# Kernel optimization log

Measured on AMD Instinct MI355X. Metric: run time of the kernel, lower is better.

Reference implementation:

```python
import jax, jax.numpy as jnp
import numpy as np

TOP_K = 2


def setup_inputs() -> dict:
    key = jax.random.key(0)
    ks = jax.random.split(key, 6)
    B, S, H, I, E = 2, 1024, 1024, 2048, 8
    s_h = 1.0 / np.sqrt(H)
    s_i = 1.0 / np.sqrt(I)
    return {
        "x": jax.random.normal(ks[0], (B, S, H), jnp.float32),
        "gate_w": jax.random.normal(ks[1], (H, E), jnp.float32) * s_h,
        "gate_b": jnp.zeros((E,), jnp.float32),
        "w1": jax.random.normal(ks[2], (E, H, I), jnp.float32) * s_h,
        "w3": jax.random.normal(ks[3], (E, H, I), jnp.float32) * s_h,
        "w2": jax.random.normal(ks[4], (E, I, H), jnp.float32) * s_i,
    }


def reference(x, gate_w, gate_b, w1, w3, w2):
    # Gating: softmax over experts, then top-k selection + renormalization.
    logits = jnp.einsum("bsh,he->bse", x, gate_w) + gate_b            # [B,S,E]
    probs = jax.nn.softmax(logits, axis=-1)
    topk_w, topk_idx = jax.lax.top_k(probs, TOP_K)                    # [B,S,K]
    topk_w = topk_w / jnp.sum(topk_w, axis=-1, keepdims=True)

    E = gate_w.shape[-1]
    # Per-token combine weight for each expert (0 if not routed there).
    # one_hot: [B,S,K,E] -> combine: [B,S,E]
    combine = jnp.sum(jax.nn.one_hot(topk_idx, E, dtype=x.dtype) * topk_w[..., None], axis=-2)

    # SwiGLU expert FFN: down(silu(gate(x)) * up(x)); dense-masked reference
    # (compute every expert on every token, weight by combine; math identical
    # to the original gather/scatter loop since combine is 0 off-route).
    out = jnp.zeros_like(x)
    for e in range(E):
        h = jax.nn.silu(x @ w1[e]) * (x @ w3[e])                      # [B,S,I]
        out = out + combine[..., e:e + 1] * (h @ w2[e])               # [B,S,H]
    return out
```

## Files before the change

kernel.cpp:

```cpp
#include <hip/hip_runtime.h>
#include <hip/hip_bf16.h>
#include <math.h>

typedef __attribute__((ext_vector_type(4))) float f32x4;
typedef __attribute__((ext_vector_type(8))) short bf16x8;

#define T_TOK 2048
#define H_DIM 1024
#define I_DIM 2048
#define E_NUM 8

__device__ inline unsigned short f2bf(float f) {
  union { float f; unsigned int u; } v; v.f = f;
  unsigned int r = v.u + 0x7fffu + ((v.u >> 16) & 1u);
  return (unsigned short)(r >> 16);
}
__device__ inline unsigned int pack2(float a, float b) {
  return (unsigned int)f2bf(a) | ((unsigned int)f2bf(b) << 16);
}

__device__ inline void gld16(const void* g, void* l) {
  __builtin_amdgcn_global_load_lds((const __attribute__((address_space(1))) void*)g,
                                   (__attribute__((address_space(3))) void*)l, 16, 0, 0);
}

__device__ inline void transpose_pair(const float* __restrict__ ip, unsigned short* __restrict__ op,
                                      int R, int C, int rp, int ct, char* smem)
{
  unsigned short (*tl)[66] = (unsigned short (*)[66])smem;
  int r0 = rp * 128, c0 = ct * 64;
  int tid = threadIdx.x;
  int rq = (tid >> 4) * 4;
  int c4 = (tid & 15) * 4;
  const float* b0 = ip + (size_t)(r0 + rq) * C + c0 + c4;
  const float* b1 = b0 + (size_t)64 * C;
  float4 v[8];
  v[0] = *(const float4*)(b0);
  v[1] = *(const float4*)(b0 + C);
  v[2] = *(const float4*)(b0 + 2 * C);
  v[3] = *(const float4*)(b0 + 3 * C);
  v[4] = *(const float4*)(b1);
  v[5] = *(const float4*)(b1 + C);
  v[6] = *(const float4*)(b1 + 2 * C);
  v[7] = *(const float4*)(b1 + 3 * C);
  const float* f = (const float*)v;
#pragma unroll
  for (int j = 0; j < 4; ++j) {
    *(unsigned int*)&tl[c4 + j][rq]          = pack2(f[0 * 4 + j], f[1 * 4 + j]);
    *(unsigned int*)&tl[c4 + j][rq + 2]      = pack2(f[2 * 4 + j], f[3 * 4 + j]);
    *(unsigned int*)&tl[64 + c4 + j][rq]     = pack2(f[4 * 4 + j], f[5 * 4 + j]);
    *(unsigned int*)&tl[64 + c4 + j][rq + 2] = pack2(f[6 * 4 + j], f[7 * 4 + j]);
  }
  __syncthreads();
  int c = tid >> 3, r8 = (tid & 7) * 8;
#pragma unroll
  for (int it = 0; it < 2; ++it) {
    int cc = c + it * 32;
#pragma unroll
    for (int p = 0; p < 2; ++p) {
      uint4 o;
      o.x = *(const unsigned int*)&tl[p * 64 + cc][r8];
      o.y = *(const unsigned int*)&tl[p * 64 + cc][r8 + 2];
      o.z = *(const unsigned int*)&tl[p * 64 + cc][r8 + 4];
      o.w = *(const unsigned int*)&tl[p * 64 + cc][r8 + 6];
      *(uint4*)(op + (size_t)(c0 + cc) * R + r0 + p * 64 + r8) = o;
    }
  }
}

__global__ __launch_bounds__(256) void gate_t13(
    const float* __restrict__ x, const float* __restrict__ gw, const float* __restrict__ gb,
    int* __restrict__ rec_e, float* __restrict__ rec_w, unsigned short* __restrict__ xb,
    const float* __restrict__ w1, const float* __restrict__ w3,
    unsigned short* __restrict__ w1t, unsigned short* __restrict__ w3t)
{
  __shared__ __align__(16) char smem[128 * 66 * 2];
  int bx = blockIdx.x;
  if (bx >= 512) {
    int idx = bx - 512;
    int m = idx >> 8;
    int t8 = idx & 255;
    int rp = t8 & 7;
    int ct = t8 >> 3;
    const float* ip = (m < 8 ? w1 : w3) + (size_t)(m & 7) * ((size_t)H_DIM * I_DIM);
    unsigned short* op = (m < 8 ? w1t : w3t) + (size_t)(m & 7) * ((size_t)H_DIM * I_DIM);
    transpose_pair(ip, op, H_DIM, I_DIM, rp, ct, smem);
    return;
  }
  int wv = threadIdx.x >> 6, lane = threadIdx.x & 63;
  int t = bx * 4 + wv;
  const float* xr = x + (size_t)t * H_DIM;
  unsigned short* xo = xb + (size_t)t * H_DIM;
  float acc[8];
#pragma unroll
  for (int e = 0; e < 8; ++e) acc[e] = 0.f;
  for (int i = 0; i < H_DIM / 64; ++i) {
    int h = i * 64 + lane;
    float xv = xr[h];
    xo[h] = f2bf(xv);
    const float4* g = (const float4*)(gw + (size_t)h * 8);
    float4 g0 = g[0], g1 = g[1];
    acc[0] += xv * g0.x; acc[1] += xv * g0.y; acc[2] += xv * g0.z; acc[3] += xv * g0.w;
    acc[4] += xv * g1.x; acc[5] += xv * g1.y; acc[6] += xv * g1.z; acc[7] += xv * g1.w;
  }
#pragma unroll
  for (int s = 1; s < 64; s <<= 1) {
#pragma unroll
    for (int e = 0; e < 8; ++e) acc[e] += __shfl_xor(acc[e], s);
  }
  if (lane == 0) {
    float l[8];
#pragma unroll
    for (int e = 0; e < 8; ++e) l[e] = acc[e] + gb[e];
    int e0 = 0;
    for (int e = 1; e < 8; ++e) if (l[e] > l[e0]) e0 = e;
    int e1 = (e0 == 0) ? 1 : 0;
    for (int e = 0; e < 8; ++e) if (e != e0 && l[e] > l[e1]) e1 = e;
    float w0 = 1.f / (1.f + expf(l[e1] - l[e0]));
    rec_e[t * 2]     = e0; rec_e[t * 2 + 1] = e1;
    rec_w[t * 2]     = w0; rec_w[t * 2 + 1] = 1.f - w0;
  }
}

__global__ __launch_bounds__(256) void route8(
    const int* __restrict__ rec_e, const float* __restrict__ rec_w,
    int* __restrict__ counts_g, int* __restrict__ list_tok, float* __restrict__ list_w)
{
  __shared__ int cnt[8];
  __shared__ int fill;
  int e = blockIdx.x;
  int tid = threadIdx.x;
  if (tid < 8) cnt[tid] = 0;
  if (tid == 0) fill = 0;
  __syncthreads();
  int e_loc[16];
  int c_loc[8];
#pragma unroll
  for (int k = 0; k < 8; ++k) c_loc[k] = 0;
#pragma unroll
  for (int it = 0; it < 16; ++it) {
    e_loc[it] = rec_e[it * 256 + tid] & 7;
    c_loc[e_loc[it]]++;
  }
#pragma unroll
  for (int k = 0; k < 8; ++k) if (c_loc[k]) atomicAdd(&cnt[k], c_loc[k]);
  __syncthreads();
  if (e == 0 && tid < 8) counts_g[tid] = cnt[tid];
  int base = 0;
#pragma unroll
  for (int k = 0; k < 8; ++k) if (k < e) base += cnt[k];
#pragma unroll
  for (int it = 0; it < 16; ++it) {
    if (e_loc[it] == e) {
      int i = it * 256 + tid;
      int pos = atomicAdd(&fill, 1);
      list_tok[base + pos] = i;
      list_w[base + pos]   = rec_w[i];
    }
  }
}

__global__ __launch_bounds__(256, 2) void gemm1_t2(
    const unsigned short* __restrict__ xb,
    const unsigned short* __restrict__ w1t,
    const unsigned short* __restrict__ w3t,
    const int* __restrict__ counts,
    const int* __restrict__ list_tok,
    unsigned short* __restrict__ hbuf,
    const float* __restrict__ w2,
    unsigned short* __restrict__ w2t)
{
  __shared__ __align__(16) char smem[49152];
  int bx = blockIdx.x;
  if (bx >= 4096) {
    int idx = bx - 4096;
    int e = idx >> 8;
    int t8 = idx & 255;
    int rp = t8 & 15;
    int ct = t8 >> 4;
    const float* ip = w2 + (size_t)e * ((size_t)H_DIM * I_DIM);
    unsigned short* op = w2t + (size_t)e * ((size_t)H_DIM * I_DIM);
    transpose_pair(ip, op, I_DIM, H_DIM, rp, ct, smem);
    return;
  }
  int e = bx >> 9;
  int y = (bx >> 4) & 31;
  int ix = bx & 15;
  int nbase = 0;
#pragma unroll
  for (int i = 0; i < 8; ++i) if (i < e) nbase += counts[i];
  int n_e = counts[e];
  int t0 = y * 128;
  if (t0 >= n_e) return;
  int i0 = ix * 128;

  int tid = threadIdx.x;
  int r2 = tid >> 2;
  int sseg = (((tid & 3) ^ (r2 & 3)) * 8);

  int sr0 = t0 + r2;       if (sr0 >= n_e) sr0 = n_e - 1;
  int sr1 = t0 + 64 + r2;  if (sr1 >= n_e) sr1 = n_e - 1;
  int tok0 = list_tok[nbase + sr0] >> 1;
  int tok1 = list_tok[nbase + sr1] >> 1;
  const char* gA0  = (const char*)(xb + (size_t)tok0 * H_DIM + sseg);
  const char* gA1  = (const char*)(xb + (size_t)tok1 * H_DIM + sseg);
  const char* gB1a = (const char*)(w1t + ((size_t)e * I_DIM + i0 + r2) * H_DIM + sseg);
  const char* gB1b = (const char*)(w1t + ((size_t)e * I_DIM + i0 + 64 + r2) * H_DIM + sseg);
  const char* gB3a = (const char*)(w3t + ((size_t)e * I_DIM + i0 + r2) * H_DIM + sseg);
  const char* gB3b = (const char*)(w3t + ((size_t)e * I_DIM + i0 + 64 + r2) * H_DIM + sseg);

#define STAGE1(buf, kb) do {                              \
    gld16(gA0  + (kb) * 2, (buf) + tid * 16);             \
    gld16(gA1  + (kb) * 2, (buf) + 4096  + tid * 16);     \
    gld16(gB1a + (kb) * 2, (buf) + 8192  + tid * 16);     \
    gld16(gB1b + (kb) * 2, (buf) + 12288 + tid * 16);     \
    gld16(gB3a + (kb) * 2, (buf) + 16384 + tid * 16);     \
    gld16(gB3b + (kb) * 2, (buf) + 20480 + tid * 16);     \
  } while (0)

  int w = tid >> 6, lane = tid & 63, lm = lane & 15, lq = lane >> 4;
  int wm = w & 1, wn = w >> 1;
  int colx = (lq ^ (lm & 3)) * 16;
  int rA = (wm * 64 + lm) * 64 + colx;
  int rB = (wn * 64 + lm) * 64 + colx;

  f32x4 acc1[4][4], acc3[4][4];
#pragma unroll
  for (int i = 0; i < 4; ++i)
#pragma unroll
    for (int j = 0; j < 4; ++j) { acc1[i][j] = (f32x4){0,0,0,0}; acc3[i][j] = (f32x4){0,0,0,0}; }

  STAGE1(smem, 0);
  __syncthreads();
  for (int kb = 0; kb < H_DIM; kb += 32) {
    char* cur = smem + (((kb >> 5) & 1) ? 24576 : 0);
    char* nxt = smem + (((kb >> 5) & 1) ? 0 : 24576);
    if (kb + 32 < H_DIM) STAGE1(nxt, kb + 32);
    bf16x8 a[4], b1[4], b3[4];
#pragma unroll
    for (int i = 0; i < 4; ++i)
      a[i] = *(const bf16x8*)(cur + rA + i * 1024);
#pragma unroll
    for (int j = 0; j < 4; ++j) {
      b1[j] = *(const bf16x8*)(cur + 8192  + rB + j * 1024);
      b3[j] = *(const bf16x8*)(cur + 16384 + rB + j * 1024);
    }
#pragma unroll
    for (int i = 0; i < 4; ++i)
#pragma unroll
      for (int j = 0; j < 4; ++j) {
        acc1[i][j] = __builtin_amdgcn_mfma_f32_16x16x32_bf16(a[i], b1[j], acc1[i][j], 0, 0, 0);
        acc3[i][j] = __builtin_amdgcn_mfma_f32_16x16x32_bf16(a[i], b3[j], acc3[i][j], 0, 0, 0);
      }
    __syncthreads();
  }
#undef STAGE1

#pragma unroll
  for (int i = 0; i < 4; ++i) {
#pragma unroll
    for (int rr = 0; rr < 4; ++rr) {
      int slot = t0 + wm * 64 + i * 16 + lq * 4 + rr;
      if (slot < n_e) {
        unsigned short* orow = hbuf + (size_t)(nbase + slot) * I_DIM + i0 + wn * 64 + lm;
#pragma unroll
        for (int j = 0; j < 4; ++j) {
          float g = acc1[i][j][rr], u = acc3[i][j][rr];
          float hv = (g / (1.f + __expf(-g))) * u;
          orow[j * 16] = f2bf(hv);
        }
      }
    }
  }
}

__global__ __launch_bounds__(256, 2) void gemm2(
    const unsigned short* __restrict__ hbuf,
    const unsigned short* __restrict__ w2t,
    const int* __restrict__ counts,
    const int* __restrict__ list_tok,
    const float* __restrict__ list_w,
    float* __restrict__ partial)
{
  __shared__ __align__(16) char smem[32768];
  int e = blockIdx.z;
  int nbase = 0;
#pragma unroll
  for (int i = 0; i < 8; ++i) if (i < e) nbase += counts[i];
  int n_e = counts[e];
  int ts = blockIdx.y >> 1, kh = blockIdx.y & 1;
  int t0 = ts * 128;
  if (t0 >= n_e) return;
  int h0 = blockIdx.x * 128;
  int k0 = kh * (I_DIM / 2);

  int tid = threadIdx.x;
  int r2 = tid >> 2;
  int sseg = (((tid & 3) ^ (r2 & 3)) * 8);

  int sr0 = t0 + r2;       if (sr0 >= n_e) sr0 = n_e - 1;
  int sr1 = t0 + 64 + r2;  if (sr1 >= n_e) sr1 = n_e - 1;
  const char* gA0 = (const char*)(hbuf + (size_t)(nbase + sr0) * I_DIM + k0 + sseg);
  const char* gA1 = (const char*)(hbuf + (size_t)(nbase + sr1) * I_DIM + k0 + sseg);
  const char* gB0 = (const char*)(w2t + ((size_t)e * H_DIM + h0 + r2) * I_DIM + k0 + sseg);
  const char* gB1 = (const char*)(w2t + ((size_t)e * H_DIM + h0 + 64 + r2) * I_DIM + k0 + sseg);

#define STAGE2(buf, kb) do {                              \
    gld16(gA0 + (kb) * 2, (buf) + tid * 16);              \
    gld16(gA1 + (kb) * 2, (buf) + 4096  + tid * 16);      \
    gld16(gB0 + (kb) * 2, (buf) + 8192  + tid * 16);      \
    gld16(gB1 + (kb) * 2, (buf) + 12288 + tid * 16);      \
  } while (0)

  int w = tid >> 6, lane = tid & 63, lm = lane & 15, lq = lane >> 4;
  int wm = w & 1, wn = w >> 1;
  int colx = (lq ^ (lm & 3)) * 16;
  int rA = (wm * 64 + lm) * 64 + colx;
  int rB = (wn * 64 + lm) * 64 + colx;

  f32x4 acc[4][4];
#pragma unroll
  for (int i = 0; i < 4; ++i)
#pragma unroll
    for (int j = 0; j < 4; ++j) acc[i][j] = (f32x4){0,0,0,0};

  STAGE2(smem, 0);
  __syncthreads();
  for (int kb = 0; kb < I_DIM / 2; kb += 32) {
    char* cur = smem + (((kb >> 5) & 1) ? 16384 : 0);
    char* nxt = smem + (((kb >> 5) & 1) ? 0 : 16384);
    if (kb + 32 < I_DIM / 2) STAGE2(nxt, kb + 32);
    bf16x8 a[4], b[4];
#pragma unroll
    for (int i = 0; i < 4; ++i)
      a[i] = *(const bf16x8*)(cur + rA + i * 1024);
#pragma unroll
    for (int j = 0; j < 4; ++j)
      b[j] = *(const bf16x8*)(cur + 8192 + rB + j * 1024);
#pragma unroll
    for (int i = 0; i < 4; ++i)
#pragma unroll
      for (int j = 0; j < 4; ++j)
        acc[i][j] = __builtin_amdgcn_mfma_f32_16x16x32_bf16(a[i], b[j], acc[i][j], 0, 0, 0);
    __syncthreads();
  }
#undef STAGE2

  int entv[4][4]; float wtv[4][4];
#pragma unroll
  for (int i = 0; i < 4; ++i)
#pragma unroll
    for (int rr = 0; rr < 4; ++rr) {
      int slot = t0 + wm * 64 + i * 16 + lq * 4 + rr;
      if (slot < n_e) { entv[i][rr] = list_tok[nbase + slot]; wtv[i][rr] = list_w[nbase + slot]; }
      else entv[i][rr] = -1;
    }
#pragma unroll
  for (int i = 0; i < 4; ++i)
#pragma unroll
    for (int j = 0; j < 4; ++j)
#pragma unroll
      for (int rr = 0; rr < 4; ++rr) {
        if (entv[i][rr] >= 0) {
          int t = entv[i][rr] >> 1, kk = entv[i][rr] & 1;
          int plane = kh * 2 + kk;
          partial[((size_t)plane * T_TOK + t) * H_DIM + h0 + wn * 64 + j * 16 + lm] =
              acc[i][j][rr] * wtv[i][rr];
        }
      }
}

__global__ __launch_bounds__(256) void combine4(const float* __restrict__ partial,
                                                float* __restrict__ out)
{
  const size_t P = (size_t)T_TOK * H_DIM;
  size_t i = (size_t)(blockIdx.x * 256 + threadIdx.x) * 4;
  float4 a = *(const float4*)(partial + i);
  float4 b = *(const float4*)(partial + P + i);
  float4 c = *(const float4*)(partial + 2 * P + i);
  float4 d = *(const float4*)(partial + 3 * P + i);
  float4 o;
  o.x = a.x + b.x + c.x + d.x;
  o.y = a.y + b.y + c.y + d.y;
  o.z = a.z + b.z + c.z + d.z;
  o.w = a.w + b.w + c.w + d.w;
  *(float4*)(out + i) = o;
}

extern "C" void kernel_launch(void* const* d_in, const int* in_sizes, int n_in,
                              void* d_out, int out_size, void* d_ws, size_t ws_size,
                              hipStream_t stream) {
  const float* x  = (const float*)d_in[0];
  const float* gw = (const float*)d_in[1];
  const float* gb = (const float*)d_in[2];
  const float* w1 = (const float*)d_in[3];
  const float* w3 = (const float*)d_in[4];
  const float* w2 = (const float*)d_in[5];
  float* out = (float*)d_out;

  char* ws = (char*)d_ws;
  int*   counts   = (int*)(ws);
  int*   rec_e    = (int*)(ws + 128);
  float* rec_w    = (float*)(ws + 16512);
  int*   list_tok = (int*)(ws + 32896);
  float* list_w   = (float*)(ws + 49280);
  const size_t MB = 1024ull * 1024ull;
  unsigned short* xb   = (unsigned short*)(ws + 1 * MB);
  unsigned short* w1t  = (unsigned short*)(ws + 5 * MB);
  float* partial       = (float*)(ws + 5 * MB);
  unsigned short* w3t  = (unsigned short*)(ws + 37 * MB);
  unsigned short* w2t  = (unsigned short*)(ws + 69 * MB);
  unsigned short* hbuf = (unsigned short*)(ws + 101 * MB);

  gate_t13<<<512 + 4096, 256, 0, stream>>>(x, gw, gb, rec_e, rec_w, xb, w1, w3, w1t, w3t);
  route8<<<8, 256, 0, stream>>>(rec_e, rec_w, counts, list_tok, list_w);
  gemm1_t2<<<4096 + 2048, 256, 0, stream>>>(xb, w1t, w3t, counts, list_tok, hbuf, w2, w2t);
  gemm2<<<dim3(H_DIM / 128, 64, E_NUM), 256, 0, stream>>>(hbuf, w2t, counts, list_tok, list_w, partial);
  combine4<<<(T_TOK * H_DIM) / (256 * 4), 256, 0, stream>>>(partial, out);
}
```

Baseline: 344.2 us.

## Triple-buffer LDS pipelines in both GEMMs and split gemm2 K four ways

Both expert GEMMs move from a double-buffered loop with two barriers per step to a three-stage LDS ring. Each stage waits with an explicit vmcnt, then takes a single barrier, and the next global-to-LDS load is issued after the fragments are read and before the MFMAs. gemm2 also splits its K dimension four ways instead of two and raises the occupancy hint to 3. That doubles the partial output planes to eight, which combine8 then sums. The goal is better latency hiding and more parallel blocks in gemm2, at the cost of more LDS per block and extra partial-buffer write and read traffic.

```diff
diff --git a/kernel.cpp b/kernel.cpp
--- a/kernel.cpp
+++ b/kernel.cpp
@@ -170,7 +170,7 @@
     const float* __restrict__ w2,
     unsigned short* __restrict__ w2t)
 {
-  __shared__ __align__(16) char smem[49152];
+  __shared__ __align__(16) char smem[73728];
   int bx = blockIdx.x;
   if (bx >= 4096) {
     int idx = bx - 4096;
@@ -230,30 +230,44 @@
 #pragma unroll
     for (int j = 0; j < 4; ++j) { acc1[i][j] = (f32x4){0,0,0,0}; acc3[i][j] = (f32x4){0,0,0,0}; }
 
+#define COMP1(cur, DOSTAGE, sbuf, skb) do {                                            \
+    bf16x8 a_[4], b1_[4], b3_[4];                                                      \
+    _Pragma("unroll") for (int i = 0; i < 4; ++i)                                      \
+      a_[i] = *(const bf16x8*)((cur) + rA + i * 1024);                                 \
+    _Pragma("unroll") for (int j = 0; j < 4; ++j) {                                    \
+      b1_[j] = *(const bf16x8*)((cur) + 8192  + rB + j * 1024);                        \
+      b3_[j] = *(const bf16x8*)((cur) + 16384 + rB + j * 1024);                        \
+    }                                                                                  \
+    if (DOSTAGE) STAGE1((sbuf), (skb));                                                \
+    _Pragma("unroll") for (int i = 0; i < 4; ++i)                                      \
+    _Pragma("unroll") for (int j = 0; j < 4; ++j) {                                    \
+      acc1[i][j] = __builtin_amdgcn_mfma_f32_16x16x32_bf16(a_[i], b1_[j], acc1[i][j], 0, 0, 0); \
+      acc3[i][j] = __builtin_amdgcn_mfma_f32_16x16x32_bf16(a_[i], b3_[j], acc3[i][j], 0, 0, 0); \
+    }                                                                                  \
+  } while (0)
+
   STAGE1(smem, 0);
-  __syncthreads();
-  for (int kb = 0; kb < H_DIM; kb += 32) {
-    char* cur = smem + (((kb >> 5) & 1) ? 24576 : 0);
-    char* nxt = smem + (((kb >> 5) & 1) ? 0 : 24576);
-    if (kb + 32 < H_DIM) STAGE1(nxt, kb + 32);
-    bf16x8 a[4], b1[4], b3[4];
-#pragma unroll
-    for (int i = 0; i < 4; ++i)
-      a[i] = *(const bf16x8*)(cur + rA + i * 1024);
-#pragma unroll
-    for (int j = 0; j < 4; ++j) {
-      b1[j] = *(const bf16x8*)(cur + 8192  + rB + j * 1024);
-      b3[j] = *(const bf16x8*)(cur + 16384 + rB + j * 1024);
-    }
-#pragma unroll
-    for (int i = 0; i < 4; ++i)
-#pragma unroll
-      for (int j = 0; j < 4; ++j) {
-        acc1[i][j] = __builtin_amdgcn_mfma_f32_16x16x32_bf16(a[i], b1[j], acc1[i][j], 0, 0, 0);
-        acc3[i][j] = __builtin_amdgcn_mfma_f32_16x16x32_bf16(a[i], b3[j], acc3[i][j], 0, 0, 0);
-      }
-    __syncthreads();
-  }
+  STAGE1(smem + 24576, 32);
+  int cb = 0;
+  for (int t = 0; t < 30; ++t) {
+    asm volatile("s_waitcnt vmcnt(6)" ::: "memory");
+    __builtin_amdgcn_sched_barrier(0);
+    __builtin_amdgcn_s_barrier();
+    char* cur = smem + cb * 24576;
+    int b2 = cb + 2; if (b2 >= 3) b2 -= 3;
+    COMP1(cur, 1, smem + b2 * 24576, (t + 2) * 32);
+    cb = (cb == 2) ? 0 : cb + 1;
+  }
+  asm volatile("s_waitcnt vmcnt(6)" ::: "memory");
+  __builtin_amdgcn_sched_barrier(0);
+  __builtin_amdgcn_s_barrier();
+  COMP1(smem + cb * 24576, 0, smem, 0);
+  cb = (cb == 2) ? 0 : cb + 1;
+  asm volatile("s_waitcnt vmcnt(0)" ::: "memory");
+  __builtin_amdgcn_sched_barrier(0);
+  __builtin_amdgcn_s_barrier();
+  COMP1(smem + cb * 24576, 0, smem, 0);
+#undef COMP1
 #undef STAGE1
 
 #pragma unroll
@@ -274,7 +288,7 @@
   }
 }
 
-__global__ __launch_bounds__(256, 2) void gemm2(
+__global__ __launch_bounds__(256, 3) void gemm2(
     const unsigned short* __restrict__ hbuf,
     const unsigned short* __restrict__ w2t,
     const int* __restrict__ counts,
@@ -282,17 +296,17 @@
     const float* __restrict__ list_w,
     float* __restrict__ partial)
 {
-  __shared__ __align__(16) char smem[32768];
+  __shared__ __align__(16) char smem[49152];
   int e = blockIdx.z;
   int nbase = 0;
 #pragma unroll
   for (int i = 0; i < 8; ++i) if (i < e) nbase += counts[i];
   int n_e = counts[e];
-  int ts = blockIdx.y >> 1, kh = blockIdx.y & 1;
+  int ts = blockIdx.y >> 2, ks = blockIdx.y & 3;
   int t0 = ts * 128;
   if (t0 >= n_e) return;
   int h0 = blockIdx.x * 128;
-  int k0 = kh * (I_DIM / 2);
+  int k0 = ks * (I_DIM / 4);
 
   int tid = threadIdx.x;
   int r2 = tid >> 2;
@@ -324,26 +338,40 @@
 #pragma unroll
     for (int j = 0; j < 4; ++j) acc[i][j] = (f32x4){0,0,0,0};
 
+#define COMP2(cur, DOSTAGE, sbuf, skb) do {                                            \
+    bf16x8 a_[4], b_[4];                                                               \
+    _Pragma("unroll") for (int i = 0; i < 4; ++i)                                      \
+      a_[i] = *(const bf16x8*)((cur) + rA + i * 1024);                                 \
+    _Pragma("unroll") for (int j = 0; j < 4; ++j)                                      \
+      b_[j] = *(const bf16x8*)((cur) + 8192 + rB + j * 1024);                          \
+    if (DOSTAGE) STAGE2((sbuf), (skb));                                                \
+    _Pragma("unroll") for (int i = 0; i < 4; ++i)                                      \
+    _Pragma("unroll") for (int j = 0; j < 4; ++j)                                      \
+      acc[i][j] = __builtin_amdgcn_mfma_f32_16x16x32_bf16(a_[i], b_[j], acc[i][j], 0, 0, 0); \
+  } while (0)
+
   STAGE2(smem, 0);
-  __syncthreads();
-  for (int kb = 0; kb < I_DIM / 2; kb += 32) {
-    char* cur = smem + (((kb >> 5) & 1) ? 16384 : 0);
-    char* nxt = smem + (((kb >> 5) & 1) ? 0 : 16384);
-    if (kb + 32 < I_DIM / 2) STAGE2(nxt, kb + 32);
-    bf16x8 a[4], b[4];
-#pragma unroll
-    for (int i = 0; i < 4; ++i)
-      a[i] = *(const bf16x8*)(cur + rA + i * 1024);
-#pragma unroll
-    for (int j = 0; j < 4; ++j)
-      b[j] = *(const bf16x8*)(cur + 8192 + rB + j * 1024);
-#pragma unroll
-    for (int i = 0; i < 4; ++i)
-#pragma unroll
-      for (int j = 0; j < 4; ++j)
-        acc[i][j] = __builtin_amdgcn_mfma_f32_16x16x32_bf16(a[i], b[j], acc[i][j], 0, 0, 0);
-    __syncthreads();
-  }
+  STAGE2(smem + 16384, 32);
+  int cb = 0;
+  for (int t = 0; t < 14; ++t) {
+    asm volatile("s_waitcnt vmcnt(4)" ::: "memory");
+    __builtin_amdgcn_sched_barrier(0);
+    __builtin_amdgcn_s_barrier();
+    char* cur = smem + cb * 16384;
+    int b2 = cb + 2; if (b2 >= 3) b2 -= 3;
+    COMP2(cur, 1, smem + b2 * 16384, (t + 2) * 32);
+    cb = (cb == 2) ? 0 : cb + 1;
+  }
+  asm volatile("s_waitcnt vmcnt(4)" ::: "memory");
+  __builtin_amdgcn_sched_barrier(0);
+  __builtin_amdgcn_s_barrier();
+  COMP2(smem + cb * 16384, 0, smem, 0);
+  cb = (cb == 2) ? 0 : cb + 1;
+  asm volatile("s_waitcnt vmcnt(0)" ::: "memory");
+  __builtin_amdgcn_sched_barrier(0);
+  __builtin_amdgcn_s_barrier();
+  COMP2(smem + cb * 16384, 0, smem, 0);
+#undef COMP2
 #undef STAGE2
 
   int entv[4][4]; float wtv[4][4];
@@ -363,27 +391,24 @@
       for (int rr = 0; rr < 4; ++rr) {
         if (entv[i][rr] >= 0) {
           int t = entv[i][rr] >> 1, kk = entv[i][rr] & 1;
-          int plane = kh * 2 + kk;
+          int plane = ks * 2 + kk;
           partial[((size_t)plane * T_TOK + t) * H_DIM + h0 + wn * 64 + j * 16 + lm] =
               acc[i][j][rr] * wtv[i][rr];
         }
       }
 }
 
-__global__ __launch_bounds__(256) void combine4(const float* __restrict__ partial,
+__global__ __launch_bounds__(256) void combine8(const float* __restrict__ partial,
                                                 float* __restrict__ out)
 {
   const size_t P = (size_t)T_TOK * H_DIM;
   size_t i = (size_t)(blockIdx.x * 256 + threadIdx.x) * 4;
-  float4 a = *(const float4*)(partial + i);
-  float4 b = *(const float4*)(partial + P + i);
-  float4 c = *(const float4*)(partial + 2 * P + i);
-  float4 d = *(const float4*)(partial + 3 * P + i);
-  float4 o;
-  o.x = a.x + b.x + c.x + d.x;
-  o.y = a.y + b.y + c.y + d.y;
-  o.z = a.z + b.z + c.z + d.z;
-  o.w = a.w + b.w + c.w + d.w;
+  float4 o = {0.f, 0.f, 0.f, 0.f};
+#pragma unroll
+  for (int p = 0; p < 8; ++p) {
+    float4 a = *(const float4*)(partial + (size_t)p * P + i);
+    o.x += a.x; o.y += a.y; o.z += a.z; o.w += a.w;
+  }
   *(float4*)(out + i) = o;
 }
 
@@ -415,6 +440,6 @@
   gate_t13<<<512 + 4096, 256, 0, stream>>>(x, gw, gb, rec_e, rec_w, xb, w1, w3, w1t, w3t);
   route8<<<8, 256, 0, stream>>>(rec_e, rec_w, counts, list_tok, list_w);
   gemm1_t2<<<4096 + 2048, 256, 0, stream>>>(xb, w1t, w3t, counts, list_tok, hbuf, w2, w2t);
-  gemm2<<<dim3(H_DIM / 128, 64, E_NUM), 256, 0, stream>>>(hbuf, w2t, counts, list_tok, list_w, partial);
-  combine4<<<(T_TOK * H_DIM) / (256 * 4), 256, 0, stream>>>(partial, out);
-}
+  gemm2<<<dim3(H_DIM / 128, 128, E_NUM), 256, 0, stream>>>(hbuf, w2t, counts, list_tok, list_w, partial);
+  combine8<<<(T_TOK * H_DIM) / (256 * 4), 256, 0, stream>>>(partial, out);
+}
```

Measured after the change: 337.9 us. No clear change (-1.8%).
